# Kernel tuning notes

Measured on AMD Instinct MI355X. Metric: run time of the kernel, lower is better.

Reference implementation:

```python
import jax, jax.numpy as jnp
import numpy as np

H = 8        # num_heads
DK = 128     # head_k_dim
DV = 128     # head_v_dim
HID = 1024   # hidden_size
CHUNK = 64   # chunk size for chunked linear attention
EPS = 1e-5


def setup_inputs() -> dict:
    key = jax.random.key(0)
    ks = jax.random.split(key, 16)
    s = 0.02
    inp = {
        "hidden_states": jax.random.normal(ks[0], (2, 8192, HID), dtype=jnp.float32),
        "Wq": jax.random.normal(ks[1], (HID, HID), dtype=jnp.float32) * s,
        "Wk": jax.random.normal(ks[2], (HID, HID), dtype=jnp.float32) * s,
        "Wv": jax.random.normal(ks[3], (HID, HID), dtype=jnp.float32) * s,
        "fmq_w1": jax.random.normal(ks[4], (DK, DK), dtype=jnp.float32) * s,
        "fmq_b1": jnp.zeros((DK,), dtype=jnp.float32),
        "fmq_w2": jax.random.normal(ks[5], (DK, DK), dtype=jnp.float32) * s,
        "fmq_b2": jnp.zeros((DK,), dtype=jnp.float32),
        "fmk_w1": jax.random.normal(ks[6], (DK, DK), dtype=jnp.float32) * s,
        "fmk_b1": jnp.zeros((DK,), dtype=jnp.float32),
        "fmk_w2": jax.random.normal(ks[7], (DK, DK), dtype=jnp.float32) * s,
        "fmk_b2": jnp.zeros((DK,), dtype=jnp.float32),
        "rms_w": jnp.ones((DV,), dtype=jnp.float32),
        "Wo": jax.random.normal(ks[8], (HID, HID), dtype=jnp.float32) * s,
    }
    return inp


def reference(hidden_states, Wq, Wk, Wv, fmq_w1, fmq_b1, fmq_w2, fmq_b2,
              fmk_w1, fmk_b1, fmk_w2, fmk_b2, rms_w, Wo):
    B, T, _ = hidden_states.shape
    scale = DK ** -0.5

    # projections (torch Linear: x @ W.T), split heads -> [B,T,H,D]
    q = (hidden_states @ Wq.T).reshape(B, T, H, DK)
    k = (hidden_states @ Wk.T).reshape(B, T, H, DK)
    v = (hidden_states @ Wv.T).reshape(B, T, H, DV)

    # Hadamard feature maps: l1(x) * l2(x)
    q = (q @ fmq_w1.T + fmq_b1) * (q @ fmq_w2.T + fmq_b2)
    k = (k @ fmk_w1.T + fmk_b1) * (k @ fmk_w2.T + fmk_b2)

    q = q * scale

    # chunked causal linear attention: o_t = q_t @ sum_{s<=t} k_s v_s^T
    N = T // CHUNK
    qc = q.reshape(B, N, CHUNK, H, DK)
    kc = k.reshape(B, N, CHUNK, H, DK)
    vc = v.reshape(B, N, CHUNK, H, DV)

    # per-chunk KV outer-product sums, exclusive prefix over chunks
    kv = jnp.einsum('bnchk,bnchv->bnhkv', kc, vc)
    S = jnp.cumsum(kv, axis=1) - kv  # state entering each chunk

    o_inter = jnp.einsum('bnchk,bnhkv->bnchv', qc, S)

    # intra-chunk causal part
    A = jnp.einsum('bnihk,bnjhk->bnhij', qc, kc)
    causal = jnp.tril(jnp.ones((CHUNK, CHUNK), dtype=bool))
    A = jnp.where(causal, A, 0.0)
    o_intra = jnp.einsum('bnhij,bnjhv->bnihv', A, vc)

    o = (o_inter + o_intra).reshape(B, T, H, DV)

    # RMSNorm over head_v_dim with affine weight
    o = o * jax.lax.rsqrt(jnp.mean(o * o, axis=-1, keepdims=True) + EPS) * rms_w

    o = o.reshape(B, T, H * DV) @ Wo.T
    return o
```

## Files before the change

### kernel.cpp

```cpp
#include <hip/hip_runtime.h>


typedef __bf16 bf16x8 __attribute__((ext_vector_type(8)));
typedef float  f32x4  __attribute__((ext_vector_type(4)));

__device__ __forceinline__ float bf2f(unsigned short u) {
  union { unsigned int i; float f; } v; v.i = ((unsigned int)u) << 16; return v.f;
}
__device__ __forceinline__ unsigned short f2bf(float f) {
  union { float f; unsigned int i; } v; v.f = f;
  return (unsigned short)((v.i + 0x8000u) >> 16);
}
__device__ __forceinline__ unsigned int pk2(float a, float b) {
  union { float f; unsigned int i; } x, y; x.f = a; y.f = b;
  return ((x.i + 0x8000u) >> 16) | ((y.i + 0x8000u) & 0xFFFF0000u);
}
__device__ __forceinline__ f32x4 mfma16(bf16x8 a, bf16x8 b, f32x4 c) {
  return __builtin_amdgcn_mfma_f32_16x16x32_bf16(a, b, c, 0, 0, 0);
}
__device__ __forceinline__ void gl_lds16(const unsigned short* g, unsigned short* l) {
  __builtin_amdgcn_global_load_lds((const __attribute__((address_space(1))) void*)g,
                                   (__attribute__((address_space(3))) void*)l, 16, 0, 0);
}

__global__ void __launch_bounds__(256)
cvt_kernel(const float* __restrict__ s, unsigned short* __restrict__ d, int n4) {
  const int i = blockIdx.x * 256 + threadIdx.x;
  if (i >= n4) return;
  const float4 f = ((const float4*)s)[i];
  uint2 o; o.x = pk2(f.x, f.y); o.y = pk2(f.z, f.w);
  ((uint2*)d)[i] = o;
}
__global__ void __launch_bounds__(256)
cvt4_kernel(const float* __restrict__ s0, const float* __restrict__ s1,
            const float* __restrict__ s2, const float* __restrict__ s3,
            unsigned short* __restrict__ d0, unsigned short* __restrict__ d1,
            unsigned short* __restrict__ d2, unsigned short* __restrict__ d3,
            int n4) {
  const int w = blockIdx.y;
  const float* s = (w == 0) ? s0 : (w == 1) ? s1 : (w == 2) ? s2 : s3;
  unsigned short* d = (w == 0) ? d0 : (w == 1) ? d1 : (w == 2) ? d2 : d3;
  const int i = blockIdx.x * 256 + threadIdx.x;
  if (i >= n4) return;
  const float4 f = ((const float4*)s)[i];
  uint2 o; o.x = pk2(f.x, f.y); o.y = pk2(f.z, f.w);
  ((uint2*)d)[i] = o;
}

__device__ __forceinline__ int stage_goff(int s) {
  const int j = s >> 3, c = (s & 7) ^ (j & 7);
  return (2 * j + (c >> 2)) * 1024 + (c & 3) * 8;
}

__device__ __forceinline__ void gemm256_loop(const unsigned short* __restrict__ gA,
                                             const unsigned short* __restrict__ gB,
                                             unsigned short* __restrict__ ldsA,
                                             unsigned short* __restrict__ ldsB,
                                             int tid, f32x4 (&acc)[8][4]) {
  const int lane = tid & 63, wid = tid >> 6;
  const int lq = lane & 15, quad = lane >> 4;
  const int wm = (wid >> 2) * 128, wn = (wid & 3) * 64;

  const unsigned short* gA0 = gA + stage_goff(tid);
  const unsigned short* gA1 = gA + stage_goff(512 + tid);
  const unsigned short* gB0 = gB + stage_goff(tid);
  const unsigned short* gB1 = gB + stage_goff(512 + tid);
  const int l0 = wid * 512;
  const int l1 = 4096 + wid * 512;
  const int soff = (lq >> 1) * 64 + (((((lq & 1) << 2) + quad) ^ ((lq >> 1) & 7))) * 8;

#pragma unroll
  for (int h = 0; h < 3; ++h) {
    gl_lds16(gA0 + h * 32, ldsA + h * 8192 + l0);
    gl_lds16(gA1 + h * 32, ldsA + h * 8192 + l1);
    gl_lds16(gB0 + h * 32, ldsB + h * 8192 + l0);
    gl_lds16(gB1 + h * 32, ldsB + h * 8192 + l1);
  }
  asm volatile("s_waitcnt vmcnt(4)" ::: "memory");
  __builtin_amdgcn_s_barrier();
  __builtin_amdgcn_sched_barrier(0);

  bf16x8 pa[2][8], pb[2][4];
#pragma unroll
  for (int f = 0; f < 8; ++f)
    pa[0][f] = *(const bf16x8*)(ldsA + (wm + f * 16) * 32 + soff);
#pragma unroll
  for (int g = 0; g < 4; ++g)
    pb[0][g] = *(const bf16x8*)(ldsB + (wn + g * 16) * 32 + soff);

#pragma unroll
  for (int u = 0; u < 32; ++u) {
    const int cur = u & 1, nxt = cur ^ 1;
    if (u > 0) {
      if (u < 30) asm volatile("s_waitcnt vmcnt(4)" ::: "memory");
      else        asm volatile("s_waitcnt vmcnt(0)" ::: "memory");
      __builtin_amdgcn_s_barrier();
      __builtin_amdgcn_sched_barrier(0);
    }
    if (u < 29) {
      unsigned short* sa = ldsA + ((u + 3) & 3) * 8192;
      unsigned short* sb = ldsB + ((u + 3) & 3) * 8192;
      gl_lds16(gA0 + (u + 3) * 32, sa + l0);
      gl_lds16(gA1 + (u + 3) * 32, sa + l1);
      gl_lds16(gB0 + (u + 3) * 32, sb + l0);
      gl_lds16(gB1 + (u + 3) * 32, sb + l1);
    }
    if (u < 31) {
      const unsigned short* An = ldsA + ((u + 1) & 3) * 8192;
      const unsigned short* Bn = ldsB + ((u + 1) & 3) * 8192;
#pragma unroll
      for (int f = 0; f < 8; ++f)
        pa[nxt][f] = *(const bf16x8*)(An + (wm + f * 16) * 32 + soff);
#pragma unroll
      for (int g = 0; g < 4; ++g)
        pb[nxt][g] = *(const bf16x8*)(Bn + (wn + g * 16) * 32 + soff);
    }
    __builtin_amdgcn_s_setprio(1);
#pragma unroll
    for (int f = 0; f < 8; ++f)
#pragma unroll
      for (int g = 0; g < 4; ++g)
        acc[f][g] = mfma16(pa[cur][f], pb[cur][g], acc[f][g]);
    __builtin_amdgcn_s_setprio(0);
  }
}

__global__ void __launch_bounds__(512, 2)
qkv_gemm256(const unsigned short* __restrict__ Xb,
            const unsigned short* __restrict__ Wqb, const unsigned short* __restrict__ Wkb,
            const unsigned short* __restrict__ Wvb,
            unsigned short* __restrict__ Q, unsigned short* __restrict__ Kf,
            unsigned short* __restrict__ VT) {
  extern __shared__ unsigned short lds[];
  const int tid = threadIdx.x;
  const int bx = blockIdx.x;
  const int tm = (bx & 7) * 8 + ((bx >> 3) & 7);
  const int ct = bx >> 6;
  const int sel = ct >> 2;
  const int rowBase = tm * 256, colBase = (ct & 3) * 256;
  const unsigned short* Bw = (sel == 0) ? Wqb : ((sel == 1) ? Wkb : Wvb);

  f32x4 acc[8][4] = {};
  gemm256_loop(Xb + (size_t)rowBase * 1024, Bw + (size_t)colBase * 1024,
               lds, lds + 32768, tid, acc);

  const int lane = tid & 63, wid = tid >> 6;
  const int lq = lane & 15, quad = lane >> 4;
  const int wm = (wid >> 2) * 128, wn = (wid & 3) * 64;
  if (sel < 2) {
    unsigned short* C = (sel == 0) ? Q : Kf;
#pragma unroll
    for (int f = 0; f < 8; ++f)
#pragma unroll
      for (int g = 0; g < 4; ++g) {
        const int col = colBase + wn + g * 16 + lq;
#pragma unroll
        for (int r = 0; r < 4; ++r) {
          const int row = rowBase + wm + f * 16 + quad * 4 + r;
          C[(size_t)row * 1024 + col] = f2bf(acc[f][g][r]);
        }
      }
  } else {
#pragma unroll
    for (int f = 0; f < 8; ++f)
#pragma unroll
      for (int g = 0; g < 4; ++g) {
        const int col = colBase + wn + g * 16 + lq;
        const int h = col >> 7, dv = col & 127;
        const int row0 = rowBase + wm + f * 16 + quad * 4;
        const int b = row0 >> 13, tl = row0 & 8191;
        ushort4 t4;
        t4.x = f2bf(acc[f][g][0]); t4.y = f2bf(acc[f][g][1]);
        t4.z = f2bf(acc[f][g][2]); t4.w = f2bf(acc[f][g][3]);
        *(ushort4*)(VT + (((size_t)(b * 8 + h) * 128 + dv) << 13) + tl) = t4;
      }
  }
}

__global__ void __launch_bounds__(512, 2)
out_gemm256(const unsigned short* __restrict__ A, const unsigned short* __restrict__ Bw,
            float* __restrict__ C) {
  extern __shared__ unsigned short lds[];
  const int tid = threadIdx.x;
  const int bx = blockIdx.x;
  const int tm = (bx & 7) * 8 + ((bx >> 3) & 7);
  const int tn = bx >> 6;
  const int rowBase = tm * 256, colBase = tn * 256;

  f32x4 acc[8][4] = {};
  gemm256_loop(A + (size_t)rowBase * 1024, Bw + (size_t)colBase * 1024,
               lds, lds + 32768, tid, acc);

  const int lane = tid & 63, wid = tid >> 6;
  const int lq = lane & 15, quad = lane >> 4;
  const int wm = (wid >> 2) * 128, wn = (wid & 3) * 64;
#pragma unroll
  for (int f = 0; f < 8; ++f)
#pragma unroll
    for (int g = 0; g < 4; ++g) {
      const int col = colBase + wn + g * 16 + lq;
#pragma unroll
      for (int r = 0; r < 4; ++r) {
        const int row = rowBase + wm + f * 16 + quad * 4 + r;
        C[(size_t)row * 1024 + col] = acc[f][g][r];
      }
    }
}

__global__ void __launch_bounds__(256)
fm_kernel(unsigned short* __restrict__ Qb, unsigned short* __restrict__ Kb,
          const unsigned short* __restrict__ fq1b, const unsigned short* __restrict__ fq2b,
          const unsigned short* __restrict__ fk1b, const unsigned short* __restrict__ fk2b,
          const float* __restrict__ fqb1, const float* __restrict__ fqb2,
          const float* __restrict__ fkb1, const float* __restrict__ fkb2) {
  __shared__ unsigned short Aq[64 * 136];
  const int z = blockIdx.z;
  unsigned short* buf = z ? Kb : Qb;
  const unsigned short* w1b = z ? fk1b : fq1b;
  const unsigned short* w2b = z ? fk2b : fq2b;
  const float* b1 = z ? fkb1 : fqb1;
  const float* b2 = z ? fkb2 : fqb2;
  const float scale = z ? 1.0f : 0.08838834764831843f;

  const int tid = threadIdx.x;
  const int t0 = blockIdx.x * 256;
  const int h = blockIdx.y, hc = h * 128;
  const int lane = tid & 63, wid = tid >> 6, lq = lane & 15, quad = lane >> 4;
  const int wn = wid * 32;

  bf16x8 w1f[4][2], w2f[4][2];
#pragma unroll
  for (int ks = 0; ks < 4; ++ks)
#pragma unroll
    for (int j = 0; j < 2; ++j) {
      const int nr = wn + j * 16 + lq;
      w1f[ks][j] = *(const bf16x8*)(w1b + nr * 128 + ks * 32 + quad * 8);
      w2f[ks][j] = *(const bf16x8*)(w2b + nr * 128 + ks * 32 + quad * 8);
    }

  const float bb1[2] = { b1[wn + lq], b1[wn + 16 + lq] };
  const float bb2[2] = { b2[wn + lq], b2[wn + 16 + lq] };

  for (int tt = 0; tt < 4; ++tt) {
    const int tb = t0 + tt * 64;
#pragma unroll
    for (int it = 0; it < 4; ++it) {
      const int p = tid + it * 256;
      const int row = p >> 4, c8 = (p & 15) * 8;
      *(uint4*)(Aq + row * 136 + c8) =
          *(const uint4*)(buf + (size_t)(tb + row) * 1024 + hc + c8);
    }
    __syncthreads();
    f32x4 a1[4][2] = {}, a2[4][2] = {};
#pragma unroll
    for (int ks = 0; ks < 4; ++ks) {
      bf16x8 af[4];
#pragma unroll
      for (int i = 0; i < 4; ++i)
        af[i] = *(const bf16x8*)(Aq + (i * 16 + lq) * 136 + ks * 32 + quad * 8);
#pragma unroll
      for (int j = 0; j < 2; ++j)
#pragma unroll
        for (int i = 0; i < 4; ++i) {
          a1[i][j] = mfma16(af[i], w1f[ks][j], a1[i][j]);
          a2[i][j] = mfma16(af[i], w2f[ks][j], a2[i][j]);
        }
    }
    __syncthreads();
#pragma unroll
    for (int j = 0; j < 2; ++j) {
      const int col = wn + j * 16 + lq;
#pragma unroll
      for (int i = 0; i < 4; ++i)
#pragma unroll
        for (int r = 0; r < 4; ++r) {
          const float v = (a1[i][j][r] + bb1[j]) * (a2[i][j][r] + bb2[j]) * scale;
          buf[(size_t)(tb + i * 16 + quad * 4 + r) * 1024 + hc + col] = f2bf(v);
        }
    }
  }
}

__global__ void __launch_bounds__(256)
kv_kernel(const unsigned short* __restrict__ Kf, const unsigned short* __restrict__ VT,
          unsigned short* __restrict__ KV) {
  __shared__ unsigned short Kt[128 * 72];
  __shared__ unsigned short Vt[128 * 72];
  const int tid = threadIdx.x;
  const int n = blockIdx.x, bh = blockIdx.y;
  const int b = bh >> 3, h = bh & 7;
  const int t0g = b * 8192 + n * 64;
  const int tl0 = n * 64;
#pragma unroll
  for (int it = 0; it < 4; ++it) {
    const int p = tid + it * 256;
    const int d = p >> 3, c8 = (p & 7) * 8;
    *(uint4*)(Vt + d * 72 + c8) =
        *(const uint4*)(VT + (((size_t)bh * 128 + d) << 13) + tl0 + c8);
    const int tok = p >> 4, c8k = (p & 15) * 8;
    const unsigned short* src = Kf + (size_t)(t0g + tok) * 1024 + h * 128 + c8k;
    ushort4 k0 = *(const ushort4*)(src);
    ushort4 k1 = *(const ushort4*)(src + 4);
    Kt[(c8k + 0) * 72 + tok] = k0.x; Kt[(c8k + 1) * 72 + tok] = k0.y;
    Kt[(c8k + 2) * 72 + tok] = k0.z; Kt[(c8k + 3) * 72 + tok] = k0.w;
    Kt[(c8k + 4) * 72 + tok] = k1.x; Kt[(c8k + 5) * 72 + tok] = k1.y;
    Kt[(c8k + 6) * 72 + tok] = k1.z; Kt[(c8k + 7) * 72 + tok] = k1.w;
  }
  __syncthreads();
  const int lane = tid & 63, wid = tid >> 6, lq = lane & 15, quad = lane >> 4;
  const int wm = (wid >> 1) * 64, wn = (wid & 1) * 64;
  f32x4 acc[4][4] = {};
#pragma unroll
  for (int ks = 0; ks < 2; ++ks) {
    bf16x8 af[4], bfr[4];
#pragma unroll
    for (int i = 0; i < 4; ++i)
      af[i] = *(const bf16x8*)(Vt + (wm + i * 16 + lq) * 72 + ks * 32 + quad * 8);
#pragma unroll
    for (int j = 0; j < 4; ++j)
      bfr[j] = *(const bf16x8*)(Kt + (wn + j * 16 + lq) * 72 + ks * 32 + quad * 8);
#pragma unroll
    for (int i = 0; i < 4; ++i)
#pragma unroll
      for (int j = 0; j < 4; ++j) acc[i][j] = mfma16(af[i], bfr[j], acc[i][j]);
  }
  const size_t base = ((size_t)bh * 128 + n) * 16384;
#pragma unroll
  for (int i = 0; i < 4; ++i)
#pragma unroll
    for (int j = 0; j < 4; ++j)
#pragma unroll
      for (int r = 0; r < 4; ++r)
        KV[base + (size_t)(wm + i * 16 + quad * 4 + r) * 128 + wn + j * 16 + lq] =
            f2bf(acc[i][j][r]);
}

__global__ void __launch_bounds__(256)
cumsum_kernel(unsigned short* __restrict__ KV) {
  const int idx = blockIdx.x * 256 + threadIdx.x;
  const int bh = idx >> 14, e = idx & 16383;
  unsigned short* p = KV + (size_t)bh * (128 * 16384) + e;
  float run = 0.f;
  for (int n = 0; n < 128; ++n) {
    const float x = bf2f(*p);
    *p = f2bf(run);
    run += x;
    p += 16384;
  }
}

__global__ void __launch_bounds__(256)
attn_kernel(const unsigned short* __restrict__ Q, const unsigned short* __restrict__ Kf,
            const unsigned short* __restrict__ VT, const unsigned short* __restrict__ S,
            const float* __restrict__ rmsw, unsigned short* __restrict__ O) {
  __shared__ uint4 smem4[3968];
  unsigned short* sm = (unsigned short*)smem4;
  unsigned short* SQ = sm;
  unsigned short* KS = sm + 8704;
  unsigned short* VTl = sm + 17920;
  unsigned short* AL = sm + 27136;
  float* OL = (float*)sm;
  float* RED = (float*)AL;
  float* SCL = RED + 256;

  const int tid = threadIdx.x;
  const int n = blockIdx.x, bh = blockIdx.y;
  const int b = bh >> 3, h = bh & 7;
  const int t0g = b * 8192 + n * 64;
  const int tl0 = n * 64;
  const int lane = tid & 63, wid = tid >> 6, lq = lane & 15, quad = lane >> 4;

#pragma unroll
  for (int it = 0; it < 4; ++it) {
    const int p = tid + it * 256;
    const int row = p >> 4, c8 = (p & 15) * 8;
    *(uint4*)(SQ + row * 136 + c8) =
        *(const uint4*)(Q + (size_t)(t0g + row) * 1024 + h * 128 + c8);
    *(uint4*)(KS + row * 136 + c8) =
        *(const uint4*)(Kf + (size_t)(t0g + row) * 1024 + h * 128 + c8);
    const int d = p >> 3, c8b = (p & 7) * 8;
    *(uint4*)(VTl + d * 72 + c8b) =
        *(const uint4*)(VT + (((size_t)bh * 128 + d) << 13) + tl0 + c8b);
  }
  __syncthreads();

  {
    f32x4 aa[4] = {};
#pragma unroll
    for (int ks = 0; ks < 4; ++ks) {
      bf16x8 kf = *(const bf16x8*)(KS + (wid * 16 + lq) * 136 + ks * 32 + quad * 8);
#pragma unroll
      for (int i = 0; i < 4; ++i) {
        bf16x8 qf = *(const bf16x8*)(SQ + (i * 16 + lq) * 136 + ks * 32 + quad * 8);
        aa[i] = mfma16(qf, kf, aa[i]);
      }
    }
#pragma unroll
    for (int i = 0; i < 4; ++i)
#pragma unroll
      for (int r = 0; r < 4; ++r) {
        const int qp = i * 16 + quad * 4 + r, kp = wid * 16 + lq;
        AL[qp * 72 + kp] = f2bf(kp <= qp ? aa[i][r] : 0.f);
      }
  }
  __syncthreads();

  const size_t sbase = ((size_t)bh * 128 + n) * 16384;
#pragma unroll
  for (int it = 0; it < 4; ++it) {
    const int p = tid + it * 256;
    const int dv = p >> 3, c8 = (p & 7) * 8;
    *(uint4*)(KS + dv * 72 + c8) = *(const uint4*)(S + sbase + (size_t)dv * 128 + c8);
  }
  __syncthreads();

  f32x4 oa[4][2] = {};
#pragma unroll
  for (int ks = 0; ks < 2; ++ks) {
    bf16x8 bv[2], sf[2];
#pragma unroll
    for (int j = 0; j < 2; ++j) {
      bv[j] = *(const bf16x8*)(VTl + (wid * 32 + j * 16 + lq) * 72 + ks * 32 + quad * 8);
      sf[j] = *(const bf16x8*)(KS + (wid * 32 + j * 16 + lq) * 72 + ks * 32 + quad * 8);
    }
#pragma unroll
    for (int i = 0; i < 4; ++i) {
      bf16x8 af = *(const bf16x8*)(AL + (i * 16 + lq) * 72 + ks * 32 + quad * 8);
      bf16x8 qf = *(const bf16x8*)(SQ + (i * 16 + lq) * 136 + ks * 32 + quad * 8);
#pragma unroll
      for (int j = 0; j < 2; ++j) {
        oa[i][j] = mfma16(af, bv[j], oa[i][j]);
        oa[i][j] = mfma16(qf, sf[j], oa[i][j]);
      }
    }
  }
  __syncthreads();

#pragma unroll
  for (int it = 0; it < 4; ++it) {
    const int p = tid + it * 256;
    const int dv = p >> 3, c8 = (p & 7) * 8;
    *(uint4*)(KS + dv * 72 + c8) =
        *(const uint4*)(S + sbase + (size_t)dv * 128 + 64 + c8);
  }
  __syncthreads();

#pragma unroll
  for (int ks = 0; ks < 2; ++ks) {
    bf16x8 sf[2];
#pragma unroll
    for (int j = 0; j < 2; ++j)
      sf[j] = *(const bf16x8*)(KS + (wid * 32 + j * 16 + lq) * 72 + ks * 32 + quad * 8);
#pragma unroll
    for (int i = 0; i < 4; ++i) {
      bf16x8 qf = *(const bf16x8*)(SQ + (i * 16 + lq) * 136 + (ks + 2) * 32 + quad * 8);
#pragma unroll
      for (int j = 0; j < 2; ++j) oa[i][j] = mfma16(qf, sf[j], oa[i][j]);
    }
  }
  __syncthreads();

#pragma unroll
  for (int i = 0; i < 4; ++i)
#pragma unroll
    for (int j = 0; j < 2; ++j)
#pragma unroll
      for (int r = 0; r < 4; ++r)
        OL[(i * 16 + quad * 4 + r) * 132 + wid * 32 + j * 16 + lq] = oa[i][j][r];
  __syncthreads();

  {
    const int r = tid >> 2, part = tid & 3;
    const float* pr = OL + r * 132 + part * 32;
    float s = 0.f;
#pragma unroll
    for (int c = 0; c < 32; ++c) { const float v = pr[c]; s += v * v; }
    RED[r * 4 + part] = s;
  }
  __syncthreads();
  if (tid < 64) {
    const float ms = (RED[tid * 4] + RED[tid * 4 + 1] + RED[tid * 4 + 2] + RED[tid * 4 + 3]) *
                     (1.f / 128.f);
    SCL[tid] = rsqrtf(ms + 1e-5f);
  }
  __syncthreads();

#pragma unroll
  for (int it = 0; it < 4; ++it) {
    const int r = (tid >> 4) + it * 16;
    const int c8 = (tid & 15) * 8;
    const float sc = SCL[r];
    unsigned short us[8];
#pragma unroll
    for (int e = 0; e < 8; ++e)
      us[e] = f2bf(OL[r * 132 + c8 + e] * sc * rmsw[c8 + e]);
    uint4 pk;
    pk.x = (unsigned int)us[0] | ((unsigned int)us[1] << 16);
    pk.y = (unsigned int)us[2] | ((unsigned int)us[3] << 16);
    pk.z = (unsigned int)us[4] | ((unsigned int)us[5] << 16);
    pk.w = (unsigned int)us[6] | ((unsigned int)us[7] << 16);
    *(uint4*)(O + (size_t)(t0g + r) * 1024 + h * 128 + c8) = pk;
  }
}

extern "C" void kernel_launch(void* const* d_in, const int* in_sizes, int n_in,
                              void* d_out, int out_size, void* d_ws, size_t ws_size,
                              hipStream_t stream) {
  const float* X    = (const float*)d_in[0];
  const float* Wq   = (const float*)d_in[1];
  const float* Wk   = (const float*)d_in[2];
  const float* Wv   = (const float*)d_in[3];
  const float* fq1  = (const float*)d_in[4];
  const float* fqb1 = (const float*)d_in[5];
  const float* fq2  = (const float*)d_in[6];
  const float* fqb2 = (const float*)d_in[7];
  const float* fk1  = (const float*)d_in[8];
  const float* fkb1 = (const float*)d_in[9];
  const float* fk2  = (const float*)d_in[10];
  const float* fkb2 = (const float*)d_in[11];
  const float* rmsw = (const float*)d_in[12];
  const float* Wo   = (const float*)d_in[13];

  static bool attr_done = false;
  if (!attr_done) {
    (void)hipFuncSetAttribute((const void*)qkv_gemm256,
                              hipFuncAttributeMaxDynamicSharedMemorySize, 131072);
    (void)hipFuncSetAttribute((const void*)out_gemm256,
                              hipFuncAttributeMaxDynamicSharedMemorySize, 131072);
    attr_done = true;
  }

  const size_t MB = 1u << 20;
  char* ws = (char*)d_ws;
  unsigned short* Q    = (unsigned short*)(ws);
  unsigned short* Kf   = (unsigned short*)(ws + 32 * MB);
  unsigned short* VT   = (unsigned short*)(ws + 64 * MB);
  unsigned short* KV   = (unsigned short*)(ws + 96 * MB);
  unsigned short* Xb   = KV;
  unsigned short* Wqb  = (unsigned short*)(ws + 160 * MB);
  unsigned short* Wkb  = (unsigned short*)(ws + 162 * MB);
  unsigned short* Wvb  = (unsigned short*)(ws + 164 * MB);
  unsigned short* Wob  = (unsigned short*)(ws + 166 * MB);
  unsigned short* fq1b = (unsigned short*)(ws + 168 * MB);
  unsigned short* fq2b = fq1b + 16384;
  unsigned short* fk1b = fq1b + 32768;
  unsigned short* fk2b = fq1b + 49152;
  unsigned short* O    = Q;

  cvt4_kernel<<<dim3(1024, 4), 256, 0, stream>>>(Wq, Wk, Wv, Wo,
                                                 Wqb, Wkb, Wvb, Wob, 262144);
  cvt4_kernel<<<dim3(16, 4), 256, 0, stream>>>(fq1, fq2, fk1, fk2,
                                               fq1b, fq2b, fk1b, fk2b, 4096);
  cvt_kernel<<<16384, 256, 0, stream>>>(X, Xb, 4194304);

  qkv_gemm256<<<dim3(768), dim3(512), 131072, stream>>>(Xb, Wqb, Wkb, Wvb, Q, Kf, VT);
  fm_kernel<<<dim3(64, 8, 2), 256, 0, stream>>>(Q, Kf, fq1b, fq2b, fk1b, fk2b,
                                                fqb1, fqb2, fkb1, fkb2);
  kv_kernel<<<dim3(128, 16), 256, 0, stream>>>(Kf, VT, KV);
  cumsum_kernel<<<1024, 256, 0, stream>>>(KV);
  attn_kernel<<<dim3(128, 16), 256, 0, stream>>>(Q, Kf, VT, KV, rmsw, O);
  out_gemm256<<<dim3(256), dim3(512), 131072, stream>>>(O, Wob, (float*)d_out);
}
```

Baseline: 411.1 us.

## Restructure QKV GEMM main loop into fine-grained phased pipeline with interleaved loads

Rewrites the 256x256 GEMM inner loop so each K step pair runs as eight phases. Each phase loads a few A fragments and, once per half, the B fragments for two K slices from LDS, issues one half-stage of global-to-LDS prefetch, and runs 16 MFMAs between two barriers. The aim is to spread global loads and LDS reads evenly across the MFMA stream instead of bursting them once per K step, and to cut register pressure by dropping the double-buffered A fragment arrays. In exchange it adds roughly twice as many barriers per K step, and the 4-slot ring now holds a ragged mix of A and B stages, so the vmcnt accounting has to stay exactly right.

```diff
diff --git a/kernel.cpp b/kernel.cpp
--- a/kernel.cpp
+++ b/kernel.cpp
@@ -69,60 +69,80 @@
   const int l1 = 4096 + wid * 512;
   const int soff = (lq >> 1) * 64 + (((((lq & 1) << 2) + quad) ^ ((lq >> 1) & 7))) * 8;
 
-#pragma unroll
-  for (int h = 0; h < 3; ++h) {
-    gl_lds16(gA0 + h * 32, ldsA + h * 8192 + l0);
-    gl_lds16(gA1 + h * 32, ldsA + h * 8192 + l1);
-    gl_lds16(gB0 + h * 32, ldsB + h * 8192 + l0);
-    gl_lds16(gB1 + h * 32, ldsB + h * 8192 + l1);
-  }
+#define STA(k) { unsigned short* d_ = ldsA + ((k) & 3) * 8192; \
+                 gl_lds16(gA0 + (k) * 32, d_ + l0); gl_lds16(gA1 + (k) * 32, d_ + l1); }
+#define STB(k) { unsigned short* d_ = ldsB + ((k) & 3) * 8192; \
+                 gl_lds16(gB0 + (k) * 32, d_ + l0); gl_lds16(gB1 + (k) * 32, d_ + l1); }
+
+  STA(0); STA(1); STB(0); STB(1); STB(2); STB(3);
   asm volatile("s_waitcnt vmcnt(4)" ::: "memory");
   __builtin_amdgcn_s_barrier();
   __builtin_amdgcn_sched_barrier(0);
 
-  bf16x8 pa[2][8], pb[2][4];
-#pragma unroll
-  for (int f = 0; f < 8; ++f)
-    pa[0][f] = *(const bf16x8*)(ldsA + (wm + f * 16) * 32 + soff);
-#pragma unroll
-  for (int g = 0; g < 4; ++g)
-    pb[0][g] = *(const bf16x8*)(ldsB + (wn + g * 16) * 32 + soff);
-
-#pragma unroll
-  for (int u = 0; u < 32; ++u) {
-    const int cur = u & 1, nxt = cur ^ 1;
-    if (u > 0) {
-      if (u < 30) asm volatile("s_waitcnt vmcnt(4)" ::: "memory");
-      else        asm volatile("s_waitcnt vmcnt(0)" ::: "memory");
-      __builtin_amdgcn_s_barrier();
-      __builtin_amdgcn_sched_barrier(0);
-    }
-    if (u < 29) {
-      unsigned short* sa = ldsA + ((u + 3) & 3) * 8192;
-      unsigned short* sb = ldsB + ((u + 3) & 3) * 8192;
-      gl_lds16(gA0 + (u + 3) * 32, sa + l0);
-      gl_lds16(gA1 + (u + 3) * 32, sa + l1);
-      gl_lds16(gB0 + (u + 3) * 32, sb + l0);
-      gl_lds16(gB1 + (u + 3) * 32, sb + l1);
-    }
-    if (u < 31) {
-      const unsigned short* An = ldsA + ((u + 1) & 3) * 8192;
-      const unsigned short* Bn = ldsB + ((u + 1) & 3) * 8192;
-#pragma unroll
-      for (int f = 0; f < 8; ++f)
-        pa[nxt][f] = *(const bf16x8*)(An + (wm + f * 16) * 32 + soff);
-#pragma unroll
-      for (int g = 0; g < 4; ++g)
-        pb[nxt][g] = *(const bf16x8*)(Bn + (wn + g * 16) * 32 + soff);
-    }
-    __builtin_amdgcn_s_setprio(1);
-#pragma unroll
-    for (int f = 0; f < 8; ++f)
-#pragma unroll
-      for (int g = 0; g < 4; ++g)
-        acc[f][g] = mfma16(pa[cur][f], pb[cur][g], acc[f][g]);
-    __builtin_amdgcn_s_setprio(0);
-  }
+  bf16x8 bfr[2][4];
+#pragma unroll
+  for (int i = 0; i < 8; ++i) {
+#pragma unroll
+    for (int half = 0; half < 2; ++half) {
+      const int ua = 4 * i + 2 * half;
+#pragma unroll
+      for (int pp = 0; pp < 4; ++pp) {
+        const int p = half * 4 + pp;
+        bf16x8 a00 = *(const bf16x8*)(ldsA + ((ua) & 3) * 8192 +
+                                      (wm + (2 * pp) * 16) * 32 + soff);
+        bf16x8 a10 = *(const bf16x8*)(ldsA + ((ua) & 3) * 8192 +
+                                      (wm + (2 * pp + 1) * 16) * 32 + soff);
+        bf16x8 a01 = *(const bf16x8*)(ldsA + ((ua + 1) & 3) * 8192 +
+                                      (wm + (2 * pp) * 16) * 32 + soff);
+        bf16x8 a11 = *(const bf16x8*)(ldsA + ((ua + 1) & 3) * 8192 +
+                                      (wm + (2 * pp + 1) * 16) * 32 + soff);
+        if (pp == 0) {
+#pragma unroll
+          for (int g = 0; g < 4; ++g) {
+            bfr[0][g] = *(const bf16x8*)(ldsB + ((ua) & 3) * 8192 +
+                                         (wn + g * 16) * 32 + soff);
+            bfr[1][g] = *(const bf16x8*)(ldsB + ((ua + 1) & 3) * 8192 +
+                                         (wn + g * 16) * 32 + soff);
+          }
+        }
+        if (p == 0) { STA(4 * i + 2); }
+        else if (p == 1) { STA(4 * i + 3); }
+        else if (i < 7) {
+          if (p == 2) { STB(4 * i + 4); }
+          else if (p == 3) { STB(4 * i + 5); }
+          else if (p == 4) { STA(4 * i + 4); }
+          else if (p == 5) { STA(4 * i + 5); }
+          else if (p == 6) { STB(4 * i + 6); }
+          else { STB(4 * i + 7); }
+        }
+        __builtin_amdgcn_s_barrier();
+        asm volatile("s_waitcnt lgkmcnt(0)" ::: "memory");
+        __builtin_amdgcn_sched_barrier(0);
+        __builtin_amdgcn_s_setprio(1);
+#pragma unroll
+        for (int g = 0; g < 4; ++g)
+          acc[2 * pp][g] = mfma16(a00, bfr[0][g], acc[2 * pp][g]);
+#pragma unroll
+        for (int g = 0; g < 4; ++g)
+          acc[2 * pp + 1][g] = mfma16(a10, bfr[0][g], acc[2 * pp + 1][g]);
+#pragma unroll
+        for (int g = 0; g < 4; ++g)
+          acc[2 * pp][g] = mfma16(a01, bfr[1][g], acc[2 * pp][g]);
+#pragma unroll
+        for (int g = 0; g < 4; ++g)
+          acc[2 * pp + 1][g] = mfma16(a11, bfr[1][g], acc[2 * pp + 1][g]);
+        __builtin_amdgcn_s_setprio(0);
+        if (pp == 3) {
+          if (i < 7) { asm volatile("s_waitcnt vmcnt(4)" ::: "memory"); }
+          else if (half == 0) { asm volatile("s_waitcnt vmcnt(0)" ::: "memory"); }
+        }
+        __builtin_amdgcn_s_barrier();
+        __builtin_amdgcn_sched_barrier(0);
+      }
+    }
+  }
+#undef STA
+#undef STB
 }
 
 __global__ void __launch_bounds__(512, 2)
```

Measured after the change: 399.8 us. 2.8% less time.
